# Kernel optimization log

Hardware: AMD Instinct MI355X
Metric: run time of the kernel (lower is better)

The kernel has to match this reference:

```python
import jax, jax.numpy as jnp
import numpy as np

N = 50000
NEG_SLOPE = 0.2  # PyG GATConv default negative_slope


def gat_conv(x, src, dst, W, a_src, a_dst, b, heads, out_dim, concat):
    # x: [N, F_in]; W: [F_in, heads*out_dim]; a_src/a_dst: [heads, out_dim]
    h = (x @ W).reshape(N, heads, out_dim)                      # [N,H,D]
    alpha_src = jnp.einsum('nhd,hd->nh', h, a_src)              # [N,H]
    alpha_dst = jnp.einsum('nhd,hd->nh', h, a_dst)              # [N,H]
    e = jax.nn.leaky_relu(alpha_src[src] + alpha_dst[dst], NEG_SLOPE)  # [E,H]
    # segment softmax over incoming edges of each destination node
    m = jax.ops.segment_max(e, dst, num_segments=N)             # [N,H]
    ex = jnp.exp(e - m[dst])
    denom = jax.ops.segment_sum(ex, dst, num_segments=N)        # [N,H]
    alpha = ex / (denom[dst] + 1e-16)                           # [E,H]
    msg = h[src] * alpha[:, :, None]                            # [E,H,D]
    out = jax.ops.segment_sum(msg, dst, num_segments=N)         # [N,H,D]
    out = out.reshape(N, heads * out_dim) if concat else out.mean(axis=1)
    return out + b


def setup_inputs() -> dict:
    key = jax.random.key(0)
    ks = jax.random.split(key, 14)
    E = 800000
    IN, HID, H, LAT = 128, 64, 4, 64

    def glorot(k, shape):
        fan = shape[0] + shape[-1]
        return jax.random.uniform(k, shape, jnp.float32, -1.0, 1.0) * np.sqrt(6.0 / fan)

    return {
        'x': jax.random.normal(ks[0], (N, IN), jnp.float32),
        'edge_index': jax.random.randint(ks[1], (2, E), 0, N, jnp.int64),
        'W1': glorot(ks[2], (IN, H * HID)),
        'a_src1': glorot(ks[3], (H, HID)),
        'a_dst1': glorot(ks[4], (H, HID)),
        'b1': jnp.zeros((H * HID,), jnp.float32),
        'W_mu': glorot(ks[5], (H * HID, LAT)),
        'a_src_mu': glorot(ks[6], (1, LAT)),
        'a_dst_mu': glorot(ks[7], (1, LAT)),
        'b_mu': jnp.zeros((LAT,), jnp.float32),
        'W_ls': glorot(ks[8], (H * HID, LAT)),
        'a_src_ls': glorot(ks[9], (1, LAT)),
        'a_dst_ls': glorot(ks[10], (1, LAT)),
        'b_ls': jnp.zeros((LAT,), jnp.float32),
    }


def reference(x, edge_index, W1, a_src1, a_dst1, b1,
              W_mu, a_src_mu, a_dst_mu, b_mu,
              W_ls, a_src_ls, a_dst_ls, b_ls):
    # PyG GATConv adds self-loops by default
    loops = jnp.arange(N, dtype=edge_index.dtype)
    src = jnp.concatenate([edge_index[0], loops])
    dst = jnp.concatenate([edge_index[1], loops])

    h = jax.nn.relu(gat_conv(x, src, dst, W1, a_src1, a_dst1, b1, 4, 64, True))
    mu = gat_conv(h, src, dst, W_mu, a_src_mu, a_dst_mu, b_mu, 1, 64, False)
    logstd = gat_conv(h, src, dst, W_ls, a_src_ls, a_dst_ls, b_ls, 1, 64, False)
    return (mu, logstd)
```

## Files before the change

kernel.cpp:

```cpp
#include <hip/hip_runtime.h>
#include <hip/hip_bf16.h>

#define NNODES 50000
#define MT 3125
#define NB 196
typedef __hip_bfloat16 bf16;
typedef __attribute__((ext_vector_type(8))) short bf16x8;
typedef __attribute__((ext_vector_type(4))) float f32x4;

__device__ __forceinline__ void unpack2(unsigned w, float& lo, float& hi){
  lo = __uint_as_float(w << 16);
  hi = __uint_as_float(w & 0xffff0000u);
}
__device__ __forceinline__ short f2bf(float f){
  union { __hip_bfloat16 h; short s; } u; u.h = __float2bfloat16(f); return u.s;
}
__device__ __forceinline__ float lrelu(float v){ return v > 0.f ? v : 0.2f * v; }

__global__ __launch_bounds__(256)
void cvt_w_k(const float* __restrict__ W1, const float* __restrict__ Wmu,
             const float* __restrict__ Wls, bf16x8* __restrict__ Bp1,
             bf16x8* __restrict__ Bp2){
  int t = blockIdx.x * 256 + threadIdx.x;
  if (t < 4096){
    int lane = t & 63, ct = (t >> 6) & 15, kt = t >> 10;
    int k0 = kt * 32 + (lane >> 4) * 8, col = ct * 16 + (lane & 15);
    bf16x8 o;
    #pragma unroll
    for (int j = 0; j < 8; j++) o[j] = f2bf(W1[(size_t)(k0 + j) * 256 + col]);
    Bp1[t] = o;
  } else if (t < 8192){
    int u = t - 4096;
    int lane = u & 63, ct = (u >> 6) & 7, kt = u >> 9;
    int k0 = kt * 32 + (lane >> 4) * 8, col = ct * 16 + (lane & 15);
    const float* W = (col < 64) ? Wmu : Wls;
    int cc = col & 63;
    bf16x8 o;
    #pragma unroll
    for (int j = 0; j < 8; j++) o[j] = f2bf(W[(size_t)(k0 + j) * 64 + cc]);
    Bp2[u] = o;
  }
}

__global__ __launch_bounds__(256)
void gemm1_mfma(const float* __restrict__ x, const bf16x8* __restrict__ Bp,
                const float* __restrict__ aS, const float* __restrict__ aD,
                bf16* __restrict__ Y, float* __restrict__ as1, float* __restrict__ ad1){
  int rt = blockIdx.x;
  int w = threadIdx.x >> 6, lane = threadIdx.x & 63;
  const float* xr = x + (size_t)(rt * 16 + (lane & 15)) * 128 + (lane >> 4) * 8;
  f32x4 z = {0.f, 0.f, 0.f, 0.f};
  f32x4 acc[4] = {z, z, z, z};
  for (int kt = 0; kt < 4; kt++){
    float4 v0 = *(const float4*)(xr + kt * 32);
    float4 v1 = *(const float4*)(xr + kt * 32 + 4);
    bf16x8 a;
    a[0] = f2bf(v0.x); a[1] = f2bf(v0.y); a[2] = f2bf(v0.z); a[3] = f2bf(v0.w);
    a[4] = f2bf(v1.x); a[5] = f2bf(v1.y); a[6] = f2bf(v1.z); a[7] = f2bf(v1.w);
    #pragma unroll
    for (int c = 0; c < 4; c++){
      bf16x8 b = Bp[(size_t)(kt * 16 + w * 4 + c) * 64 + lane];
      acc[c] = __builtin_amdgcn_mfma_f32_16x16x32_bf16(a, b, acc[c], 0, 0, 0);
    }
  }
  int row0 = rt * 16 + (lane >> 4) * 4;
  #pragma unroll
  for (int c = 0; c < 4; c++){
    int col = w * 64 + c * 16 + (lane & 15);
    #pragma unroll
    for (int i = 0; i < 4; i++)
      Y[(size_t)(row0 + i) * 256 + col] = __float2bfloat16(acc[c][i]);
  }
  float aSv[4], aDv[4];
  #pragma unroll
  for (int c = 0; c < 4; c++){
    int col = c * 16 + (lane & 15);
    aSv[c] = aS[w * 64 + col];
    aDv[c] = aD[w * 64 + col];
  }
  #pragma unroll
  for (int i = 0; i < 4; i++){
    float s1 = 0.f, s2 = 0.f;
    #pragma unroll
    for (int c = 0; c < 4; c++){
      s1 = fmaf(acc[c][i], aSv[c], s1);
      s2 = fmaf(acc[c][i], aDv[c], s2);
    }
    #pragma unroll
    for (int o = 1; o < 16; o <<= 1){
      s1 += __shfl_xor(s1, o);
      s2 += __shfl_xor(s2, o);
    }
    if ((lane & 15) == 0){
      int node = row0 + i;
      as1[node * 4 + w] = s1;
      ad1[node * 4 + w] = s2;
    }
  }
}

__global__ __launch_bounds__(256)
void gemm2_mfma(const bf16x8* __restrict__ Ap, const bf16x8* __restrict__ Bp,
                const float* __restrict__ aSmu, const float* __restrict__ aDmu,
                const float* __restrict__ aSls, const float* __restrict__ aDls,
                bf16* __restrict__ Ymu, bf16* __restrict__ Yls,
                float* __restrict__ as2m, float* __restrict__ ad2m,
                float* __restrict__ as2l, float* __restrict__ ad2l){
  int w = threadIdx.x >> 6, lane = threadIdx.x & 63;
  int rt = blockIdx.x * 4 + w;
  if (rt >= MT) return;
  f32x4 z = {0.f, 0.f, 0.f, 0.f};
  f32x4 acc[8] = {z, z, z, z, z, z, z, z};
  for (int kt = 0; kt < 8; kt++){
    bf16x8 a = Ap[(size_t)(rt * 8 + kt) * 64 + lane];
    #pragma unroll
    for (int c = 0; c < 8; c++){
      bf16x8 b = Bp[(size_t)(kt * 8 + c) * 64 + lane];
      acc[c] = __builtin_amdgcn_mfma_f32_16x16x32_bf16(a, b, acc[c], 0, 0, 0);
    }
  }
  int row0 = rt * 16 + (lane >> 4) * 4;
  #pragma unroll
  for (int c = 0; c < 4; c++){
    int col = c * 16 + (lane & 15);
    #pragma unroll
    for (int i = 0; i < 4; i++){
      Ymu[(size_t)(row0 + i) * 64 + col] = __float2bfloat16(acc[c][i]);
      Yls[(size_t)(row0 + i) * 64 + col] = __float2bfloat16(acc[4 + c][i]);
    }
  }
  float aSm[4], aDm[4], aSl[4], aDl[4];
  #pragma unroll
  for (int c = 0; c < 4; c++){
    int col = c * 16 + (lane & 15);
    aSm[c] = aSmu[col]; aDm[c] = aDmu[col];
    aSl[c] = aSls[col]; aDl[c] = aDls[col];
  }
  #pragma unroll
  for (int i = 0; i < 4; i++){
    float s1 = 0.f, s2 = 0.f, s3 = 0.f, s4 = 0.f;
    #pragma unroll
    for (int c = 0; c < 4; c++){
      s1 = fmaf(acc[c][i], aSm[c], s1);
      s2 = fmaf(acc[c][i], aDm[c], s2);
      s3 = fmaf(acc[4 + c][i], aSl[c], s3);
      s4 = fmaf(acc[4 + c][i], aDl[c], s4);
    }
    #pragma unroll
    for (int o = 1; o < 16; o <<= 1){
      s1 += __shfl_xor(s1, o);
      s2 += __shfl_xor(s2, o);
      s3 += __shfl_xor(s3, o);
      s4 += __shfl_xor(s4, o);
    }
    if ((lane & 15) == 0){
      int node = row0 + i;
      as2m[node] = s1; ad2m[node] = s2;
      as2l[node] = s3; ad2l[node] = s4;
    }
  }
}

__global__ __launch_bounds__(256)
void bhist_k(const int* __restrict__ ei, int E0, int Etot, int* __restrict__ bcnt){
  __shared__ int lh[NB];
  for (int i = threadIdx.x; i < NB; i += 256) lh[i] = 0;
  __syncthreads();
  int base = blockIdx.x * 1024 + threadIdx.x;
  #pragma unroll
  for (int q = 0; q < 4; q++){
    int e = base + q * 256;
    if (e < Etot){
      int d = (e < E0) ? ei[E0 + e] : e - E0;
      atomicAdd(&lh[d >> 8], 1);
    }
  }
  __syncthreads();
  for (int i = threadIdx.x; i < NB; i += 256)
    if (lh[i]) atomicAdd(&bcnt[i], lh[i]);
}

__global__ __launch_bounds__(256)
void bscan_k(const int* __restrict__ bcnt, int* __restrict__ bbase,
             int* __restrict__ bcur, int total){
  __shared__ int buf[256];
  int t = threadIdx.x;
  int v = (t < NB) ? bcnt[t] : 0;
  buf[t] = v; __syncthreads();
  int acc = v;
  for (int off = 1; off < 256; off <<= 1){
    int x = (t >= off) ? buf[t - off] : 0;
    __syncthreads();
    acc += x; buf[t] = acc; __syncthreads();
  }
  if (t < NB){ int ex = acc - v; bbase[t] = ex; bcur[t] = ex; }
  if (t == 0) bbase[NB] = total;
}

__global__ __launch_bounds__(256)
void bscat_k(const int* __restrict__ ei, int E0, int Etot,
             int* __restrict__ bcur, unsigned* __restrict__ buck){
  __shared__ int lh[NB];
  __shared__ int lbase[NB];
  for (int i = threadIdx.x; i < NB; i += 256) lh[i] = 0;
  __syncthreads();
  int base = blockIdx.x * 1024 + threadIdx.x;
  int sA[4], dA[4], rA[4];
  #pragma unroll
  for (int q = 0; q < 4; q++){
    int e = base + q * 256;
    sA[q] = -1;
    if (e < Etot){
      int s, d;
      if (e < E0){ s = ei[e]; d = ei[E0 + e]; } else { s = d = e - E0; }
      sA[q] = s; dA[q] = d;
      rA[q] = atomicAdd(&lh[d >> 8], 1);
    }
  }
  __syncthreads();
  for (int i = threadIdx.x; i < NB; i += 256)
    lbase[i] = lh[i] ? atomicAdd(&bcur[i], lh[i]) : 0;
  __syncthreads();
  #pragma unroll
  for (int q = 0; q < 4; q++){
    if (sA[q] >= 0){
      int bk = dA[q] >> 8;
      buck[lbase[bk] + rA[q]] = ((unsigned)(dA[q] & 255) << 16) | (unsigned)sA[q];
    }
  }
}

__global__ __launch_bounds__(256)
void bcsr_k(const unsigned* __restrict__ buck, const int* __restrict__ bbase,
            int* __restrict__ offs, int* __restrict__ srcs, int n){
  int b = blockIdx.x;
  int lo = bbase[b], hi = bbase[b + 1];
  __shared__ int eh[256];
  __shared__ int buf[256];
  int t = threadIdx.x;
  eh[t] = 0;
  __syncthreads();
  for (int j = lo + t; j < hi; j += 256)
    atomicAdd(&eh[(buck[j] >> 16) & 255], 1);
  __syncthreads();
  int v = eh[t];
  buf[t] = v; __syncthreads();
  int acc = v;
  for (int off = 1; off < 256; off <<= 1){
    int x = (t >= off) ? buf[t - off] : 0;
    __syncthreads();
    acc += x; buf[t] = acc; __syncthreads();
  }
  int loff = acc - v;
  int node = b * 256 + t;
  if (node < n) offs[node] = lo + loff;
  if (b == NB - 1 && t == 0) offs[n] = bbase[NB];
  __syncthreads();
  eh[t] = loff;
  __syncthreads();
  for (int j = lo + t; j < hi; j += 256){
    unsigned val = buck[j];
    int dlo = (val >> 16) & 255;
    int rank = atomicAdd(&eh[dlo], 1);
    srcs[lo + rank] = (int)(val & 0xffffu);
  }
}

__global__ __launch_bounds__(256)
void gat_aggr1_k(const int* __restrict__ offs, const int* __restrict__ srcs,
                 const float* __restrict__ as, const float* __restrict__ ad,
                 const bf16* __restrict__ h, const float* __restrict__ b,
                 bf16x8* __restrict__ Ap2, int n){
  int node = blockIdx.x * 4 + (threadIdx.x >> 6);
  if (node >= n) return;
  int lane = threadIdx.x & 63;
  int beg = offs[node], end = offs[node + 1];
  int hP   = (lane >> 3) & 3;
  int oct  = lane & 7;
  int slot = lane >> 5;
  float advP = ad[node * 4 + hP];
  float m = -1e30f, s = 0.f;
  float acc[8];
  #pragma unroll
  for (int i = 0; i < 8; i++) acc[i] = 0.f;
  #pragma unroll 4
  for (int j0 = beg; j0 < end; j0 += 2){
    int j = j0 + slot;
    if (j < end){
      int si = srcs[j];
      float e = lrelu(as[si * 4 + hP] + advP);
      float p;
      if (e > m){
        float f = __expf(m - e);
        s = s * f + 1.f;
        #pragma unroll
        for (int i = 0; i < 8; i++) acc[i] *= f;
        m = e; p = 1.f;
      } else {
        p = __expf(e - m);
        s += p;
      }
      uint4 dw = *(const uint4*)(h + (size_t)si * 256 + hP * 64 + oct * 8);
      float lo, hi;
      unpack2(dw.x, lo, hi); acc[0] = fmaf(lo, p, acc[0]); acc[1] = fmaf(hi, p, acc[1]);
      unpack2(dw.y, lo, hi); acc[2] = fmaf(lo, p, acc[2]); acc[3] = fmaf(hi, p, acc[3]);
      unpack2(dw.z, lo, hi); acc[4] = fmaf(lo, p, acc[4]); acc[5] = fmaf(hi, p, acc[5]);
      unpack2(dw.w, lo, hi); acc[6] = fmaf(lo, p, acc[6]); acc[7] = fmaf(hi, p, acc[7]);
    }
  }
  {
    float mo = __shfl_xor(m, 32);
    float so = __shfl_xor(s, 32);
    float nm = fmaxf(m, mo);
    float f  = __expf(m - nm);
    float fo = __expf(mo - nm);
    s = s * f + so * fo;
    #pragma unroll
    for (int i = 0; i < 8; i++)
      acc[i] = acc[i] * f + __shfl_xor(acc[i], 32) * fo;
  }
  if (lane < 32){
    float inv = 1.f / (s + 1e-16f);
    bf16x8 o;
    #pragma unroll
    for (int i = 0; i < 8; i++){
      float vv = acc[i] * inv + b[lane * 8 + i];
      o[i] = f2bf(vv > 0.f ? vv : 0.f);
    }
    int kt = lane >> 2, g = lane & 3;
    int rt = node >> 4, r = node & 15;
    Ap2[(size_t)(rt * 8 + kt) * 64 + g * 16 + r] = o;
  }
}

__global__ __launch_bounds__(256)
void gat_aggr2_k(const int* __restrict__ offs, const int* __restrict__ srcs,
                 const float* __restrict__ as2m, const float* __restrict__ ad2m,
                 const float* __restrict__ as2l, const float* __restrict__ ad2l,
                 const bf16* __restrict__ hmu, const bf16* __restrict__ hls,
                 const float* __restrict__ bmu, const float* __restrict__ bls,
                 float* __restrict__ outmu, float* __restrict__ outls, int n){
  int node = blockIdx.x * 4 + (threadIdx.x >> 6);
  if (node >= n) return;
  int lane = threadIdx.x & 63;
  int beg = offs[node], end = offs[node + 1];
  int br   = (lane >> 3) & 1;
  int oct  = lane & 7;
  int slot = lane >> 4;
  const float* asP = br ? as2l : as2m;
  float advP = (br ? ad2l : ad2m)[node];
  const bf16* hP = br ? hls : hmu;
  float m = -1e30f, s = 0.f;
  float acc[8];
  #pragma unroll
  for (int i = 0; i < 8; i++) acc[i] = 0.f;
  #pragma unroll 4
  for (int j0 = beg; j0 < end; j0 += 4){
    int j = j0 + slot;
    if (j < end){
      int si = srcs[j];
      float e = lrelu(asP[si] + advP);
      float p;
      if (e > m){
        float f = __expf(m - e);
        s = s * f + 1.f;
        #pragma unroll
        for (int i = 0; i < 8; i++) acc[i] *= f;
        m = e; p = 1.f;
      } else {
        p = __expf(e - m);
        s += p;
      }
      uint4 dw = *(const uint4*)(hP + (size_t)si * 64 + oct * 8);
      float lo, hi;
      unpack2(dw.x, lo, hi); acc[0] = fmaf(lo, p, acc[0]); acc[1] = fmaf(hi, p, acc[1]);
      unpack2(dw.y, lo, hi); acc[2] = fmaf(lo, p, acc[2]); acc[3] = fmaf(hi, p, acc[3]);
      unpack2(dw.z, lo, hi); acc[4] = fmaf(lo, p, acc[4]); acc[5] = fmaf(hi, p, acc[5]);
      unpack2(dw.w, lo, hi); acc[6] = fmaf(lo, p, acc[6]); acc[7] = fmaf(hi, p, acc[7]);
    }
  }
  #pragma unroll
  for (int off = 16; off <= 32; off <<= 1){
    float mo = __shfl_xor(m, off);
    float so = __shfl_xor(s, off);
    float nm = fmaxf(m, mo);
    float f  = __expf(m - nm);
    float fo = __expf(mo - nm);
    s = s * f + so * fo;
    #pragma unroll
    for (int i = 0; i < 8; i++)
      acc[i] = acc[i] * f + __shfl_xor(acc[i], off) * fo;
    m = nm;
  }
  if (lane < 16){
    float inv = 1.f / (s + 1e-16f);
    const float* bb = (lane >= 8) ? bls : bmu;
    float* out = (lane >= 8) ? outls : outmu;
    float v[8];
    #pragma unroll
    for (int i = 0; i < 8; i++) v[i] = acc[i] * inv + bb[oct * 8 + i];
    float* op = out + (size_t)node * 64 + oct * 8;
    *(float4*)op       = make_float4(v[0], v[1], v[2], v[3]);
    *(float4*)(op + 4) = make_float4(v[4], v[5], v[6], v[7]);
  }
}

extern "C" void kernel_launch(void* const* d_in, const int* in_sizes, int n_in,
                              void* d_out, int out_size, void* d_ws, size_t ws_size,
                              hipStream_t stream){
  const float* x    = (const float*)d_in[0];
  const int*   ei   = (const int*)d_in[1];
  const float* W1   = (const float*)d_in[2];
  const float* aS1  = (const float*)d_in[3];
  const float* aD1  = (const float*)d_in[4];
  const float* b1   = (const float*)d_in[5];
  const float* Wmu  = (const float*)d_in[6];
  const float* aSmu = (const float*)d_in[7];
  const float* aDmu = (const float*)d_in[8];
  const float* bmu  = (const float*)d_in[9];
  const float* Wls  = (const float*)d_in[10];
  const float* aSls = (const float*)d_in[11];
  const float* aDls = (const float*)d_in[12];
  const float* bls  = (const float*)d_in[13];

  const int N    = NNODES;
  const int E0   = in_sizes[1] / 2;
  const int Etot = E0 + N;

  float* ws = (float*)d_ws;
  bf16x8* Ap2  = (bf16x8*)(ws);
  bf16*   h1bf = (bf16*)(ws + 6400000);
  bf16*   h2mu = (bf16*)(ws + 12800000);
  bf16*   h2ls = (bf16*)(ws + 14400000);
  float*  as1  = ws + 16000000;
  float*  ad1  = ws + 16200000;
  float*  as2m = ws + 16400000;
  float*  ad2m = ws + 16450000;
  float*  as2l = ws + 16500000;
  float*  ad2l = ws + 16550000;
  int*      offs  = (int*)(ws + 16600000);
  int*      srcs  = (int*)(ws + 16650016);
  unsigned* buck  = (unsigned*)(ws + 17500016);
  int*      bcnt  = (int*)(ws + 18350016);
  int*      bbase = (int*)(ws + 18350272);
  int*      bcur  = (int*)(ws + 18350544);
  bf16x8*   Bp1   = (bf16x8*)(ws + 18351040);
  bf16x8*   Bp2   = (bf16x8*)(ws + 18367424);

  float* outmu = (float*)d_out;
  float* outls = (float*)d_out + 3200000;

  const int egrid4 = (Etot + 1023) / 1024;

  hipMemsetAsync(bcnt, 0, 256 * sizeof(int), stream);
  bhist_k<<<egrid4, 256, 0, stream>>>(ei, E0, Etot, bcnt);
  bscan_k<<<1, 256, 0, stream>>>(bcnt, bbase, bcur, Etot);
  bscat_k<<<egrid4, 256, 0, stream>>>(ei, E0, Etot, bcur, buck);
  bcsr_k<<<NB, 256, 0, stream>>>(buck, bbase, offs, srcs, N);

  cvt_w_k<<<32, 256, 0, stream>>>(W1, Wmu, Wls, Bp1, Bp2);

  gemm1_mfma<<<MT, 256, 0, stream>>>(x, Bp1, aS1, aD1, h1bf, as1, ad1);
  gat_aggr1_k<<<(N + 3) / 4, 256, 0, stream>>>(offs, srcs, as1, ad1, h1bf, b1, Ap2, N);

  gemm2_mfma<<<(MT + 3) / 4, 256, 0, stream>>>(Ap2, Bp2, aSmu, aDmu, aSls, aDls,
                                               h2mu, h2ls, as2m, ad2m, as2l, ad2l);
  gat_aggr2_k<<<(N + 3) / 4, 256, 0, stream>>>(offs, srcs, as2m, ad2m, as2l, ad2l,
                                               h2mu, h2ls, bmu, bls, outmu, outls, N);
}
```

Before: 241.3 us.

## Replace online softmax with two-pass max-then-accumulate in GAT aggregation kernels

Both aggregation kernels now run a first pass over each node's incoming edges to compute the per-head max logit with a wave reduction. The second pass then accumulates exp(e - max) without the branchy online rescaling of the accumulators, and the cross-slot merge becomes a plain sum. Blocks shrink from 4 waves to 2 and the unroll in aggr1 grows. This removes divergent rescale branches and extra exps, at the cost of re-reading srcs and attention scores per edge.

```diff
diff --git a/kernel.cpp b/kernel.cpp
--- a/kernel.cpp
+++ b/kernel.cpp
@@ -266,40 +266,37 @@
   }
 }
 
-__global__ __launch_bounds__(256)
+__global__ __launch_bounds__(128)
 void gat_aggr1_k(const int* __restrict__ offs, const int* __restrict__ srcs,
                  const float* __restrict__ as, const float* __restrict__ ad,
                  const bf16* __restrict__ h, const float* __restrict__ b,
                  bf16x8* __restrict__ Ap2, int n){
-  int node = blockIdx.x * 4 + (threadIdx.x >> 6);
+  int node = blockIdx.x * 2 + (threadIdx.x >> 6);
   if (node >= n) return;
   int lane = threadIdx.x & 63;
   int beg = offs[node], end = offs[node + 1];
-  int hP   = (lane >> 3) & 3;
-  int oct  = lane & 7;
-  int slot = lane >> 5;
-  float advP = ad[node * 4 + hP];
-  float m = -1e30f, s = 0.f;
+  int hA = lane >> 4, iA = lane & 15;
+  float advA = ad[node * 4 + hA];
+  float m = -1e30f;
+  for (int j = beg + iA; j < end; j += 16)
+    m = fmaxf(m, lrelu(as[srcs[j] * 4 + hA] + advA));
+  #pragma unroll
+  for (int o = 1; o < 16; o <<= 1) m = fmaxf(m, __shfl_xor(m, o));
+  int hP = (lane >> 3) & 3, oct = lane & 7, slot = lane >> 5;
+  float mP   = __shfl(m, hP * 16);
+  float advP = __shfl(advA, hP * 16);
+  float s = 0.f;
   float acc[8];
   #pragma unroll
   for (int i = 0; i < 8; i++) acc[i] = 0.f;
-  #pragma unroll 4
+  #pragma unroll 8
   for (int j0 = beg; j0 < end; j0 += 2){
     int j = j0 + slot;
     if (j < end){
       int si = srcs[j];
       float e = lrelu(as[si * 4 + hP] + advP);
-      float p;
-      if (e > m){
-        float f = __expf(m - e);
-        s = s * f + 1.f;
-        #pragma unroll
-        for (int i = 0; i < 8; i++) acc[i] *= f;
-        m = e; p = 1.f;
-      } else {
-        p = __expf(e - m);
-        s += p;
-      }
+      float p = __expf(e - mP);
+      s += p;
       uint4 dw = *(const uint4*)(h + (size_t)si * 256 + hP * 64 + oct * 8);
       float lo, hi;
       unpack2(dw.x, lo, hi); acc[0] = fmaf(lo, p, acc[0]); acc[1] = fmaf(hi, p, acc[1]);
@@ -308,17 +305,9 @@
       unpack2(dw.w, lo, hi); acc[6] = fmaf(lo, p, acc[6]); acc[7] = fmaf(hi, p, acc[7]);
     }
   }
-  {
-    float mo = __shfl_xor(m, 32);
-    float so = __shfl_xor(s, 32);
-    float nm = fmaxf(m, mo);
-    float f  = __expf(m - nm);
-    float fo = __expf(mo - nm);
-    s = s * f + so * fo;
-    #pragma unroll
-    for (int i = 0; i < 8; i++)
-      acc[i] = acc[i] * f + __shfl_xor(acc[i], 32) * fo;
-  }
+  s += __shfl_xor(s, 32);
+  #pragma unroll
+  for (int i = 0; i < 8; i++) acc[i] += __shfl_xor(acc[i], 32);
   if (lane < 32){
     float inv = 1.f / (s + 1e-16f);
     bf16x8 o;
@@ -333,24 +322,31 @@
   }
 }
 
-__global__ __launch_bounds__(256)
+__global__ __launch_bounds__(128)
 void gat_aggr2_k(const int* __restrict__ offs, const int* __restrict__ srcs,
                  const float* __restrict__ as2m, const float* __restrict__ ad2m,
                  const float* __restrict__ as2l, const float* __restrict__ ad2l,
                  const bf16* __restrict__ hmu, const bf16* __restrict__ hls,
                  const float* __restrict__ bmu, const float* __restrict__ bls,
                  float* __restrict__ outmu, float* __restrict__ outls, int n){
-  int node = blockIdx.x * 4 + (threadIdx.x >> 6);
+  int node = blockIdx.x * 2 + (threadIdx.x >> 6);
   if (node >= n) return;
   int lane = threadIdx.x & 63;
   int beg = offs[node], end = offs[node + 1];
-  int br   = (lane >> 3) & 1;
-  int oct  = lane & 7;
-  int slot = lane >> 4;
+  const float* asA = (lane >= 32) ? as2l : as2m;
+  float advA = ((lane >= 32) ? ad2l : ad2m)[node];
+  int iA = lane & 31;
+  float m = -1e30f;
+  for (int j = beg + iA; j < end; j += 32)
+    m = fmaxf(m, lrelu(asA[srcs[j]] + advA));
+  #pragma unroll
+  for (int o = 1; o < 32; o <<= 1) m = fmaxf(m, __shfl_xor(m, o));
+  int br = (lane >> 3) & 1, oct = lane & 7, slot = lane >> 4;
+  float mP   = __shfl(m, br * 32);
+  float advP = __shfl(advA, br * 32);
   const float* asP = br ? as2l : as2m;
-  float advP = (br ? ad2l : ad2m)[node];
-  const bf16* hP = br ? hls : hmu;
-  float m = -1e30f, s = 0.f;
+  const bf16*  hP  = br ? hls : hmu;
+  float s = 0.f;
   float acc[8];
   #pragma unroll
   for (int i = 0; i < 8; i++) acc[i] = 0.f;
@@ -360,17 +356,8 @@
     if (j < end){
       int si = srcs[j];
       float e = lrelu(asP[si] + advP);
-      float p;
-      if (e > m){
-        float f = __expf(m - e);
-        s = s * f + 1.f;
-        #pragma unroll
-        for (int i = 0; i < 8; i++) acc[i] *= f;
-        m = e; p = 1.f;
-      } else {
-        p = __expf(e - m);
-        s += p;
-      }
+      float p = __expf(e - mP);
+      s += p;
       uint4 dw = *(const uint4*)(hP + (size_t)si * 64 + oct * 8);
       float lo, hi;
       unpack2(dw.x, lo, hi); acc[0] = fmaf(lo, p, acc[0]); acc[1] = fmaf(hi, p, acc[1]);
@@ -381,16 +368,9 @@
   }
   #pragma unroll
   for (int off = 16; off <= 32; off <<= 1){
-    float mo = __shfl_xor(m, off);
-    float so = __shfl_xor(s, off);
-    float nm = fmaxf(m, mo);
-    float f  = __expf(m - nm);
-    float fo = __expf(mo - nm);
-    s = s * f + so * fo;
-    #pragma unroll
-    for (int i = 0; i < 8; i++)
-      acc[i] = acc[i] * f + __shfl_xor(acc[i], off) * fo;
-    m = nm;
+    s += __shfl_xor(s, off);
+    #pragma unroll
+    for (int i = 0; i < 8; i++) acc[i] += __shfl_xor(acc[i], off);
   }
   if (lane < 16){
     float inv = 1.f / (s + 1e-16f);
@@ -461,10 +441,10 @@
   cvt_w_k<<<32, 256, 0, stream>>>(W1, Wmu, Wls, Bp1, Bp2);
 
   gemm1_mfma<<<MT, 256, 0, stream>>>(x, Bp1, aS1, aD1, h1bf, as1, ad1);
-  gat_aggr1_k<<<(N + 3) / 4, 256, 0, stream>>>(offs, srcs, as1, ad1, h1bf, b1, Ap2, N);
+  gat_aggr1_k<<<(N + 1) / 2, 128, 0, stream>>>(offs, srcs, as1, ad1, h1bf, b1, Ap2, N);
 
   gemm2_mfma<<<(MT + 3) / 4, 256, 0, stream>>>(Ap2, Bp2, aSmu, aDmu, aSls, aDls,
                                                h2mu, h2ls, as2m, ad2m, as2l, ad2l);
-  gat_aggr2_k<<<(N + 3) / 4, 256, 0, stream>>>(offs, srcs, as2m, ad2m, as2l, ad2l,
+  gat_aggr2_k<<<(N + 1) / 2, 128, 0, stream>>>(offs, srcs, as2m, ad2m, as2l, ad2l,
                                                h2mu, h2ls, bmu, bls, outmu, outls, N);
 }
```

Result: faster. 231.5 us (-4.1%).
